# Kernel tuning notes

Hardware: AMD Instinct MI355X
Metric: run time of the kernel (lower is better)

## Reference

```python
import jax, jax.numpy as jnp
import numpy as np

B, N, A = 32, 1024, 256          # batch, n_entities, n_agents
D_IN, D_H, H = 256, 256, 8       # input_dim, hidden_dim, n_heads
SCALE = 1.0 / np.sqrt(D_H)
EPS = 1e-12


def setup_inputs() -> dict:
    key = jax.random.key(0)
    ks = jax.random.split(key, 7)
    x = jax.random.normal(ks[0], (B, N, D_IN), dtype=jnp.float32)
    # binary visibility mask [batch, n_agents, n_entities]
    m = (jax.random.uniform(ks[1], (B, A, N)) > 0.5).astype(jnp.float32)
    # encoder Linear(input_dim, hidden_dim): weight [out,in], bias [out]
    W_enc = jax.random.normal(ks[2], (D_H, D_IN), dtype=jnp.float32) / np.sqrt(D_IN)
    b_enc = jnp.zeros((D_H,), dtype=jnp.float32)
    # per-head projection matrices stacked [H, D_H, D_H] (torch.randn init)
    WQ = jax.random.normal(ks[3], (H, D_H, D_H), dtype=jnp.float32)
    WK = jax.random.normal(ks[4], (H, D_H, D_H), dtype=jnp.float32)
    WV = jax.random.normal(ks[5], (H, D_H, D_H), dtype=jnp.float32)
    return {"x": x, "m": m, "W_enc": W_enc, "b_enc": b_enc, "WQ": WQ, "WK": WK, "WV": WV}


def reference(x, m, W_enc, b_enc, WQ, WK, WV):
    # encode: LeakyReLU then Linear
    h = jnp.einsum('bni,oi->bno', jax.nn.leaky_relu(x), W_enc) + b_enc  # [B,N,D_H]
    n_agents = m.shape[1]
    ha = h[:, :n_agents]                                   # [B,A,D_H]
    # per-head projections, heads vectorized
    Q = jnp.einsum('bad,hde->bhae', ha, WQ)                # [B,H,A,D_H]
    K = jnp.einsum('bnd,hde->bhne', h, WK)                 # [B,H,N,D_H]
    V = jnp.einsum('bnd,hde->bhne', h, WV)                 # [B,H,N,D_H]
    S = jnp.einsum('bhae,bhne->bhan', Q, K) * SCALE        # [B,H,A,N]
    P = jax.nn.softmax(S, axis=-1)
    P = P * m[:, None]                                     # post-softmax mask
    prob = P / (jnp.sum(P, axis=-1, keepdims=True) + EPS)  # renormalize
    z = jnp.einsum('bhan,bhne->bhae', prob, V)             # [B,H,A,D_H]
    return jnp.mean(z, axis=1)                             # [B,A,D_H]
```

## Files before the change

kernel.cpp:

```cpp
#include <hip/hip_runtime.h>
#include <math.h>

namespace {
constexpr int B_N  = 32;
constexpr int SEQ  = 1024;
constexpr int AG   = 256;
constexpr int D    = 256;
constexpr int NH   = 8;
constexpr float SCALE = 0.0625f;
constexpr float EPS   = 1e-12f;

constexpr size_t HHI_OFF  = 0;
constexpr size_t HLO_OFF  = 16777216;
constexpr size_t HT_OFF   = 33554432;
constexpr size_t MTHI_OFF = 50331648;
constexpr size_t MTLO_OFF = 51380224;
constexpr size_t MB_OFF   = 52428800;
constexpr size_t WVT_OFF  = 53477376;
constexpr size_t Z16_OFF  = 54525952;
}

typedef __attribute__((ext_vector_type(8))) short short8;
typedef __attribute__((ext_vector_type(4))) float floatx4;
#define MFMA_BF(A,B,C) __builtin_amdgcn_mfma_f32_16x16x32_bf16(A,B,C,0,0,0)

__device__ __forceinline__ unsigned short bf16_rtne(float f) {
    unsigned u = __float_as_uint(f);
    u += 0x7fffu + ((u >> 16) & 1u);
    return (unsigned short)(u >> 16);
}
__device__ __forceinline__ float bf16_tof(unsigned short h) {
    return __uint_as_float(((unsigned)h) << 16);
}
__device__ __forceinline__ void async16(void* lds, const void* g) {
    __builtin_amdgcn_global_load_lds(
        (const __attribute__((address_space(1))) unsigned int*)g,
        (__attribute__((address_space(3))) unsigned int*)lds,
        16, 0, 0);
}

__global__ __launch_bounds__(256) void enc_kernel(
    const float* __restrict__ x, const float* __restrict__ W_enc,
    const float* __restrict__ b_enc,
    ushort* __restrict__ h_hi, ushort* __restrict__ h_lo)
{
    __shared__ float AsT[32][68];
    __shared__ float BsT[32][68];
    const int t  = threadIdx.x;
    const int tx = t & 15, ty = t >> 4;
    const int col0 = blockIdx.x * 64;
    const int row0 = blockIdx.y * 64;

    float acc[4][4];
#pragma unroll
    for (int r = 0; r < 4; ++r)
#pragma unroll
        for (int c = 0; c < 4; ++c) acc[r][c] = 0.f;

    for (int k0 = 0; k0 < 256; k0 += 32) {
        __syncthreads();
#pragma unroll
        for (int ss = 0; ss < 2; ++ss) {
            int flat = t + 256 * ss;
            int rr = flat >> 3, k4 = flat & 7;
            float4 v = *(const float4*)(x + (size_t)(row0 + rr) * 256 + k0 + k4 * 4);
            v.x = v.x > 0.f ? v.x : 0.01f * v.x;
            v.y = v.y > 0.f ? v.y : 0.01f * v.y;
            v.z = v.z > 0.f ? v.z : 0.01f * v.z;
            v.w = v.w > 0.f ? v.w : 0.01f * v.w;
            AsT[k4*4+0][rr] = v.x; AsT[k4*4+1][rr] = v.y;
            AsT[k4*4+2][rr] = v.z; AsT[k4*4+3][rr] = v.w;
            float4 wv = *(const float4*)(W_enc + (size_t)(col0 + rr) * 256 + k0 + k4 * 4);
            BsT[k4*4+0][rr] = wv.x; BsT[k4*4+1][rr] = wv.y;
            BsT[k4*4+2][rr] = wv.z; BsT[k4*4+3][rr] = wv.w;
        }
        __syncthreads();
#pragma unroll 8
        for (int kk = 0; kk < 32; ++kk) {
            float4 a4 = *(const float4*)&AsT[kk][ty * 4];
            float4 b4 = *(const float4*)&BsT[kk][tx * 4];
            const float ar[4] = {a4.x, a4.y, a4.z, a4.w};
            const float bc[4] = {b4.x, b4.y, b4.z, b4.w};
#pragma unroll
            for (int r = 0; r < 4; ++r)
#pragma unroll
                for (int c = 0; c < 4; ++c)
                    acc[r][c] = fmaf(ar[r], bc[c], acc[r][c]);
        }
    }

    float4 bv = *(const float4*)(b_enc + col0 + tx * 4);
    const float bb4[4] = {bv.x, bv.y, bv.z, bv.w};
#pragma unroll
    for (int r = 0; r < 4; ++r) {
        const int row = row0 + ty * 4 + r;
        ushort hi4[4], lo4[4];
#pragma unroll
        for (int c = 0; c < 4; ++c) {
            float v = acc[r][c] + bb4[c];
            hi4[c] = bf16_rtne(v);
            lo4[c] = bf16_rtne(v - bf16_tof(hi4[c]));
        }
        *(ushort4*)(h_hi + (size_t)row * 256 + col0 + tx * 4) =
            make_ushort4(hi4[0], hi4[1], hi4[2], hi4[3]);
        *(ushort4*)(h_lo + (size_t)row * 256 + col0 + tx * 4) =
            make_ushort4(lo4[0], lo4[1], lo4[2], lo4[3]);
    }
}

__global__ __launch_bounds__(256) void prep_fused(
    const float* __restrict__ m, unsigned* __restrict__ mb,
    const ushort* __restrict__ h_hi, ushort* __restrict__ hT,
    const float* __restrict__ WV, ushort* __restrict__ WVt,
    const float* __restrict__ WQ, const float* __restrict__ WK,
    ushort* __restrict__ Mt_hi, ushort* __restrict__ Mt_lo)
{
    __shared__ __align__(16) char plds[17408];
    const int t = threadIdx.x;
    const int v = blockIdx.x;

    if (v < 1024) {
        const int idx = v * 256 + t;
        const float4* src = (const float4*)(m + (size_t)idx * 32);
        unsigned wbits = 0;
#pragma unroll
        for (int i = 0; i < 8; ++i) {
            float4 vv = src[i];
            wbits |= (vv.x > 0.5f ? 1u : 0u) << (i * 4 + 0);
            wbits |= (vv.y > 0.5f ? 1u : 0u) << (i * 4 + 1);
            wbits |= (vv.z > 0.5f ? 1u : 0u) << (i * 4 + 2);
            wbits |= (vv.w > 0.5f ? 1u : 0u) << (i * 4 + 3);
        }
        mb[idx] = wbits;
    } else if (v < 3072) {
        ushort (*T)[72] = (ushort(*)[72])plds;
        const int v1 = v - 1024;
        const int n0 = (v1 & 15) * 64, d0 = ((v1 >> 4) & 3) * 64, b = v1 >> 6;
        {
            const int r = t >> 2, c = (t & 3) * 16;
            const ushort* src = h_hi + ((size_t)(b * 1024 + n0 + r)) * 256 + d0 + c;
            *(short8*)&T[r][c]     = *(const short8*)src;
            *(short8*)&T[r][c + 8] = *(const short8*)(src + 8);
        }
        __syncthreads();
        {
            const int dd = t >> 2, seg = (t & 3) * 16;
            ushort tmp[16];
#pragma unroll
            for (int j = 0; j < 16; ++j) tmp[j] = T[seg + j][dd];
            ushort* dst = hT + ((size_t)(b * 256 + d0 + dd)) * 1024 + n0 + seg;
            *(short8*)dst       = *(short8*)&tmp[0];
            *(short8*)(dst + 8) = *(short8*)&tmp[8];
        }
    } else if (v < 3200) {
        float (*T)[68] = (float(*)[68])plds;
        const int v2 = v - 3072;
        const int d0 = (v2 & 3) * 64, e0 = ((v2 >> 2) & 3) * 64, h = v2 >> 4;
        {
            const int r = t >> 2, c = (t & 3) * 16;
            const float* src = WV + ((size_t)(h * 256 + d0 + r)) * 256 + e0 + c;
#pragma unroll
            for (int j = 0; j < 4; ++j)
                *(float4*)&T[r][c + j * 4] = *(const float4*)(src + j * 4);
        }
        __syncthreads();
        {
            const int ee = t >> 2, seg = (t & 3) * 16;
            ushort tmp[16];
#pragma unroll
            for (int j = 0; j < 16; ++j) tmp[j] = bf16_rtne(T[seg + j][ee]);
            ushort* dst = WVt + ((size_t)(h * 256 + e0 + ee)) * 256 + d0 + seg;
            *(short8*)dst       = *(short8*)&tmp[0];
            *(short8*)(dst + 8) = *(short8*)&tmp[8];
        }
    } else {
        float (*AsT)[68] = (float(*)[68])plds;
        float (*BsT)[68] = (float(*)[68])(plds + 8704);
        const int v3 = v - 3200;
        const int tx = t & 15, ty = t >> 4;
        const int col0 = (v3 & 3) * 64;
        const int row0 = ((v3 >> 2) & 3) * 64;
        const int hz   = v3 >> 4;
        const float* A  = WK + (size_t)hz * 256 * 256;
        const float* Bm = WQ + (size_t)hz * 256 * 256;
        ushort* Chi = Mt_hi + (size_t)hz * 256 * 256;
        ushort* Clo = Mt_lo + (size_t)hz * 256 * 256;

        float acc[4][4];
#pragma unroll
        for (int r = 0; r < 4; ++r)
#pragma unroll
            for (int c = 0; c < 4; ++c) acc[r][c] = 0.f;

        for (int k0 = 0; k0 < 256; k0 += 32) {
            __syncthreads();
#pragma unroll
            for (int ss = 0; ss < 2; ++ss) {
                int flat = t + 256 * ss;
                int rr = flat >> 3, k4 = flat & 7;
                float4 vv = *(const float4*)(A + (size_t)(row0 + rr) * 256 + k0 + k4 * 4);
                AsT[k4*4+0][rr] = vv.x; AsT[k4*4+1][rr] = vv.y;
                AsT[k4*4+2][rr] = vv.z; AsT[k4*4+3][rr] = vv.w;
                float4 wv = *(const float4*)(Bm + (size_t)(col0 + rr) * 256 + k0 + k4 * 4);
                BsT[k4*4+0][rr] = wv.x; BsT[k4*4+1][rr] = wv.y;
                BsT[k4*4+2][rr] = wv.z; BsT[k4*4+3][rr] = wv.w;
            }
            __syncthreads();
#pragma unroll 8
            for (int kk = 0; kk < 32; ++kk) {
                float4 a4 = *(const float4*)&AsT[kk][ty * 4];
                float4 b4 = *(const float4*)&BsT[kk][tx * 4];
                const float ar[4] = {a4.x, a4.y, a4.z, a4.w};
                const float bc[4] = {b4.x, b4.y, b4.z, b4.w};
#pragma unroll
                for (int r = 0; r < 4; ++r)
#pragma unroll
                    for (int c = 0; c < 4; ++c)
                        acc[r][c] = fmaf(ar[r], bc[c], acc[r][c]);
            }
        }
#pragma unroll
        for (int r = 0; r < 4; ++r) {
            const int row = row0 + ty * 4 + r;
            ushort hi4[4], lo4[4];
#pragma unroll
            for (int c = 0; c < 4; ++c) {
                float vv = acc[r][c];
                hi4[c] = bf16_rtne(vv);
                lo4[c] = bf16_rtne(vv - bf16_tof(hi4[c]));
            }
            *(ushort4*)(Chi + (size_t)row * 256 + col0 + tx * 4) =
                make_ushort4(hi4[0], hi4[1], hi4[2], hi4[3]);
            *(ushort4*)(Clo + (size_t)row * 256 + col0 + tx * 4) =
                make_ushort4(lo4[0], lo4[1], lo4[2], lo4[3]);
        }
    }
}

__global__ __launch_bounds__(512, 2) void attn_mfma(
    const ushort* __restrict__ h_hi, const ushort* __restrict__ h_lo,
    const ushort* __restrict__ hT,   const ushort* __restrict__ Mt_hi,
    const ushort* __restrict__ Mt_lo, const unsigned* __restrict__ mbits,
    ushort* __restrict__ zout)
{
    __shared__ __align__(16) char lds[108544];
    ushort* pP = (ushort*)(lds + 98304);

    const int t    = threadIdx.x;
    const int wv   = t >> 6;
    const int lane = t & 63;
    const int l15  = lane & 15;
    const int quad = lane >> 4;
    const int f    = blockIdx.x;
    const int b    = (f & 7) + 8 * (f >> 7);
    const int mid  = (f >> 3) & 15;
    const int hh   = (mid >> 2) * 2 + (wv >> 2);
    const int a0   = (mid & 3) * 64;
    const int aw   = a0 + (wv & 3) * 16;

    const ushort* hbh = h_hi + (size_t)b * SEQ * D;
    const ushort* hbl = h_lo + (size_t)b * SEQ * D;
    const ushort* hTb = hT   + (size_t)b * D * SEQ;

    floatx4 qac[16];
#pragma unroll
    for (int i = 0; i < 16; ++i) qac[i] = (floatx4){0.f, 0.f, 0.f, 0.f};

    for (int kc = 0; kc < 4; ++kc) {
        short8 Ah[2], Al[2];
#pragma unroll
        for (int kt = 0; kt < 2; ++kt) {
            const size_t ao = ((size_t)b * SEQ + aw + l15) * D +
                              kc * 64 + kt * 32 + quad * 8;
            Ah[kt] = *(const short8*)(h_hi + ao);
            Al[kt] = *(const short8*)(h_lo + ao);
        }
#pragma unroll
        for (int nt2 = 0; nt2 < 16; ++nt2) {
#pragma unroll
            for (int kt = 0; kt < 2; ++kt) {
                const size_t mo = ((size_t)hh * D + nt2 * 16 + l15) * D +
                                  kc * 64 + kt * 32 + quad * 8;
                short8 Bh = *(const short8*)(Mt_hi + mo);
                short8 Bl = *(const short8*)(Mt_lo + mo);
                qac[nt2] = MFMA_BF(Ah[kt], Bh, qac[nt2]);
                qac[nt2] = MFMA_BF(Al[kt], Bh, qac[nt2]);
                qac[nt2] = MFMA_BF(Ah[kt], Bl, qac[nt2]);
            }
        }
    }

    short8 Qhi[8], Qlo[8];
    {
        float* qscr = (float*)lds;
        for (int c = 0; c < 4; ++c) {
#pragma unroll
            for (int j = 0; j < 4; ++j)
#pragma unroll
                for (int r = 0; r < 4; ++r)
                    qscr[(wv * 16 + quad * 4 + r) * 68 + j * 16 + l15] = qac[c * 4 + j][r];
#pragma unroll
            for (int kt = 0; kt < 2; ++kt) {
                const float* pr = &qscr[(wv * 16 + l15) * 68 + kt * 32 + quad * 8];
                float ftmp[8];
                *(float4*)&ftmp[0] = *(const float4*)pr;
                *(float4*)&ftmp[4] = *(const float4*)(pr + 4);
                short8 hi, lo;
#pragma unroll
                for (int e = 0; e < 8; ++e) {
                    unsigned short hb = bf16_rtne(ftmp[e]);
                    hi[e] = (short)hb;
                    lo[e] = (short)bf16_rtne(ftmp[e] - bf16_tof(hb));
                }
                Qhi[c * 2 + kt] = hi;
                Qlo[c * 2 + kt] = lo;
            }
        }
    }
    __syncthreads();

    auto issue_tile = [&](char* buf, int n0) {
        ushort* dh = (ushort*)buf;
        ushort* dl = (ushort*)(buf + 16384);
        ushort* dT = (ushort*)(buf + 32768);
#pragma unroll
        for (int i = 0; i < 2; ++i) {
            const int slot = wv * 128 + i * 64 + lane;
            const int row  = slot >> 5;
            const int p    = slot & 31;
            const int c    = p ^ (row & 7);
            const size_t go = (size_t)(n0 + row) * 256 + c * 8;
            const size_t lo_ = (size_t)(wv * 128 + i * 64) * 8;
            async16(dh + lo_, hbh + go);
            async16(dl + lo_, hbl + go);
        }
#pragma unroll
        for (int i = 0; i < 2; ++i) {
            const int slot = wv * 128 + i * 64 + lane;
            const int row  = slot >> 2;
            const int p    = slot & 3;
            const int c    = p ^ ((row >> 2) & 3);
            async16(dT + (size_t)(wv * 128 + i * 64) * 8,
                    hTb + (size_t)row * 1024 + n0 + c * 8);
        }
    };

    issue_tile(lds,         0);
    issue_tile(lds + 49152, 32);
    __syncthreads();

    floatx4 zac[16];
#pragma unroll
    for (int i = 0; i < 16; ++i) zac[i] = (floatx4){0.f, 0.f, 0.f, 0.f};
    float mx[4] = {-INFINITY, -INFINITY, -INFINITY, -INFINITY};
    float Za[4] = {0.f, 0.f, 0.f, 0.f};
    float Zm[4] = {0.f, 0.f, 0.f, 0.f};

    for (int nt = 0; nt < 32; ++nt) {
        const int n0 = nt * 32;
        char* cur = lds + (size_t)(nt & 1) * 49152;
        ushort* hS_hi = (ushort*)cur;
        ushort* hS_lo = (ushort*)(cur + 16384);
        ushort* hTS   = (ushort*)(cur + 32768);

        floatx4 sac[2];
        sac[0] = (floatx4){0.f, 0.f, 0.f, 0.f};
        sac[1] = (floatx4){0.f, 0.f, 0.f, 0.f};
#pragma unroll
        for (int ks = 0; ks < 8; ++ks) {
            const int cg = ks * 4 + quad;
#pragma unroll
            for (int ntile = 0; ntile < 2; ++ntile) {
                const int row = ntile * 16 + l15;
                const int off = row * 256 + (cg ^ (row & 7)) * 8;
                short8 Bh = *(const short8*)&hS_hi[off];
                short8 Bl = *(const short8*)&hS_lo[off];
                sac[ntile] = MFMA_BF(Qhi[ks], Bh, sac[ntile]);
                sac[ntile] = MFMA_BF(Qlo[ks], Bh, sac[ntile]);
                sac[ntile] = MFMA_BF(Qhi[ks], Bl, sac[ntile]);
            }
        }

        float alr[4];
#pragma unroll
        for (int r = 0; r < 4; ++r) {
            const int a = aw + quad * 4 + r;
            const unsigned w0 = mbits[((size_t)b * AG + a) * (SEQ / 32) + nt];
            float l0 = sac[0][r] * SCALE, l1 = sac[1][r] * SCALE;
            float mt = fmaxf(l0, l1);
#pragma unroll
            for (int off = 1; off < 16; off <<= 1) mt = fmaxf(mt, __shfl_xor(mt, off));
            const float mxn = fmaxf(mx[r], mt);
            const float al  = __expf(mx[r] - mxn);
            float e0 = __expf(l0 - mxn), e1 = __expf(l1 - mxn);
            float p0 = ((w0 >> l15) & 1u)        ? e0 : 0.f;
            float p1 = ((w0 >> (16 + l15)) & 1u) ? e1 : 0.f;
            float za = e0 + e1;
            float zm = p0 + p1;
#pragma unroll
            for (int off = 1; off < 16; off <<= 1) {
                za += __shfl_xor(za, off);
                zm += __shfl_xor(zm, off);
            }
            Za[r] = Za[r] * al + za;
            Zm[r] = Zm[r] * al + zm;
            mx[r] = mxn;
            pP[(wv * 16 + quad * 4 + r) * 40 + l15]      = bf16_rtne(p0);
            pP[(wv * 16 + quad * 4 + r) * 40 + 16 + l15] = bf16_rtne(p1);
            alr[r] = al;
        }
#pragma unroll
        for (int dt = 0; dt < 16; ++dt) {
            zac[dt][0] *= alr[0]; zac[dt][1] *= alr[1];
            zac[dt][2] *= alr[2]; zac[dt][3] *= alr[3];
        }

        short8 Pf = *(const short8*)&pP[(wv * 16 + l15) * 40 + quad * 8];
#pragma unroll
        for (int dt = 0; dt < 16; ++dt) {
            const int row = dt * 16 + l15;
            const int p   = quad ^ ((row >> 2) & 3);
            short8 Bf = *(const short8*)&hTS[row * 32 + p * 8];
            zac[dt] = MFMA_BF(Pf, Bf, zac[dt]);
        }

        __syncthreads();
        if (nt + 2 < 32) issue_tile(cur, (nt + 2) * 32);
    }

#pragma unroll
    for (int r = 0; r < 4; ++r) {
        const int a = aw + quad * 4 + r;
        const float inv = 1.0f / (Zm[r] + EPS * Za[r]);
        ushort* zr = zout + (((size_t)b * NH + hh) * AG + a) * D;
#pragma unroll
        for (int dt = 0; dt < 16; ++dt)
            zr[dt * 16 + l15] = bf16_rtne(zac[dt][r] * inv);
    }
}

__global__ __launch_bounds__(256) void out_mfma(
    const ushort* __restrict__ z16, const ushort* __restrict__ WVt,
    float* __restrict__ out)
{
    const int t    = threadIdx.x;
    const int wv   = t >> 6;
    const int lane = t & 63;
    const int l15  = lane & 15;
    const int quad = lane >> 4;
    const int e0 = blockIdx.x * 64;
    const int a0 = blockIdx.y * 64;
    const int b  = blockIdx.z;
    const int aw = a0 + wv * 16;

    floatx4 acc[4];
#pragma unroll
    for (int i = 0; i < 4; ++i) acc[i] = (floatx4){0.f, 0.f, 0.f, 0.f};

#pragma unroll 4
    for (int c = 0; c < 64; ++c) {
        const int hh = c >> 3, d0 = (c & 7) * 32;
        short8 Af = *(const short8*)(z16 +
            (((size_t)b * NH + hh) * AG + aw + l15) * D + d0 + quad * 8);
#pragma unroll
        for (int et = 0; et < 4; ++et) {
            short8 Bf = *(const short8*)(WVt +
                ((size_t)hh * D + e0 + et * 16 + l15) * D + d0 + quad * 8);
            acc[et] = MFMA_BF(Af, Bf, acc[et]);
        }
    }
#pragma unroll
    for (int et = 0; et < 4; ++et)
#pragma unroll
        for (int r = 0; r < 4; ++r)
            out[((size_t)b * AG + aw + quad * 4 + r) * D + e0 + et * 16 + l15] =
                acc[et][r] * 0.125f;
}

extern "C" void kernel_launch(void* const* d_in, const int* in_sizes, int n_in,
                              void* d_out, int out_size, void* d_ws, size_t ws_size,
                              hipStream_t stream)
{
    (void)in_sizes; (void)n_in; (void)out_size; (void)ws_size;
    const float* x     = (const float*)d_in[0];
    const float* m     = (const float*)d_in[1];
    const float* W_enc = (const float*)d_in[2];
    const float* b_enc = (const float*)d_in[3];
    const float* WQ    = (const float*)d_in[4];
    const float* WK    = (const float*)d_in[5];
    const float* WV    = (const float*)d_in[6];
    float* out = (float*)d_out;
    char* ws = (char*)d_ws;

    ushort*   h_hi  = (ushort*)(ws + HHI_OFF);
    ushort*   h_lo  = (ushort*)(ws + HLO_OFF);
    ushort*   hT    = (ushort*)(ws + HT_OFF);
    ushort*   Mt_hi = (ushort*)(ws + MTHI_OFF);
    ushort*   Mt_lo = (ushort*)(ws + MTLO_OFF);
    unsigned* mbits = (unsigned*)(ws + MB_OFF);
    ushort*   WVt   = (ushort*)(ws + WVT_OFF);
    ushort*   z16   = (ushort*)(ws + Z16_OFF);

    enc_kernel<<<dim3(4, 512, 1), dim3(256), 0, stream>>>(
        x, W_enc, b_enc, h_hi, h_lo);
    prep_fused<<<dim3(3328, 1, 1), dim3(256), 0, stream>>>(
        m, mbits, h_hi, hT, WV, WVt, WQ, WK, Mt_hi, Mt_lo);
    attn_mfma<<<dim3(512, 1, 1), dim3(512), 0, stream>>>(
        h_hi, h_lo, hT, Mt_hi, Mt_lo, mbits, z16);
    out_mfma<<<dim3(4, 4, B_N), dim3(256), 0, stream>>>(z16, WVt, out);
}
```

Baseline: 585.9 us.

## Shrink attention blocks to one head, single-buffer K tile, read hT from global

Each attention block now covers one head with 4 waves (256 threads) instead of two heads with 8 waves, and 1024 blocks are launched. The K tile is single-buffered, and the next tile's load is issued mid-iteration after the score MFMAs. The V-side hT operand is read straight from global memory instead of being staged in LDS. LDS use drops from about 106KB to 37KB so more blocks can be resident, at the cost of uncached global V loads per MFMA and weaker copy/compute overlap.

```diff
diff --git a/kernel.cpp b/kernel.cpp
--- a/kernel.cpp
+++ b/kernel.cpp
@@ -237,14 +237,14 @@
     }
 }
 
-__global__ __launch_bounds__(512, 2) void attn_mfma(
+__global__ __launch_bounds__(256, 3) void attn_mfma(
     const ushort* __restrict__ h_hi, const ushort* __restrict__ h_lo,
     const ushort* __restrict__ hT,   const ushort* __restrict__ Mt_hi,
     const ushort* __restrict__ Mt_lo, const unsigned* __restrict__ mbits,
     ushort* __restrict__ zout)
 {
-    __shared__ __align__(16) char lds[108544];
-    ushort* pP = (ushort*)(lds + 98304);
+    __shared__ __align__(16) char lds[37888];
+    ushort* pP = (ushort*)(lds + 32768);
 
     const int t    = threadIdx.x;
     const int wv   = t >> 6;
@@ -252,11 +252,11 @@
     const int l15  = lane & 15;
     const int quad = lane >> 4;
     const int f    = blockIdx.x;
-    const int b    = (f & 7) + 8 * (f >> 7);
-    const int mid  = (f >> 3) & 15;
-    const int hh   = (mid >> 2) * 2 + (wv >> 2);
-    const int a0   = (mid & 3) * 64;
-    const int aw   = a0 + (wv & 3) * 16;
+    const int b    = (f & 7) + 8 * (f >> 8);
+    const int rk   = (f >> 3) & 31;
+    const int hh   = rk >> 2;
+    const int a0   = (rk & 3) * 64;
+    const int aw   = a0 + wv * 16;
 
     const ushort* hbh = h_hi + (size_t)b * SEQ * D;
     const ushort* hbl = h_lo + (size_t)b * SEQ * D;
@@ -319,34 +319,23 @@
     }
     __syncthreads();
 
-    auto issue_tile = [&](char* buf, int n0) {
-        ushort* dh = (ushort*)buf;
-        ushort* dl = (ushort*)(buf + 16384);
-        ushort* dT = (ushort*)(buf + 32768);
-#pragma unroll
-        for (int i = 0; i < 2; ++i) {
-            const int slot = wv * 128 + i * 64 + lane;
+    auto issue_tile = [&](int n0) {
+        ushort* dh = (ushort*)lds;
+        ushort* dl = (ushort*)(lds + 16384);
+#pragma unroll
+        for (int i = 0; i < 4; ++i) {
+            const int slot = wv * 256 + i * 64 + lane;
             const int row  = slot >> 5;
             const int p    = slot & 31;
             const int c    = p ^ (row & 7);
-            const size_t go = (size_t)(n0 + row) * 256 + c * 8;
-            const size_t lo_ = (size_t)(wv * 128 + i * 64) * 8;
+            const size_t go  = (size_t)(n0 + row) * 256 + c * 8;
+            const size_t lo_ = (size_t)(wv * 256 + i * 64) * 8;
             async16(dh + lo_, hbh + go);
             async16(dl + lo_, hbl + go);
         }
-#pragma unroll
-        for (int i = 0; i < 2; ++i) {
-            const int slot = wv * 128 + i * 64 + lane;
-            const int row  = slot >> 2;
-            const int p    = slot & 3;
-            const int c    = p ^ ((row >> 2) & 3);
-            async16(dT + (size_t)(wv * 128 + i * 64) * 8,
-                    hTb + (size_t)row * 1024 + n0 + c * 8);
-        }
     };
 
-    issue_tile(lds,         0);
-    issue_tile(lds + 49152, 32);
+    issue_tile(0);
     __syncthreads();
 
     floatx4 zac[16];
@@ -356,12 +345,13 @@
     float Za[4] = {0.f, 0.f, 0.f, 0.f};
     float Zm[4] = {0.f, 0.f, 0.f, 0.f};
 
+    const unsigned* mbr = mbits + ((size_t)b * AG + aw + quad * 4) * (SEQ / 32);
+    const ushort*   hTl = hTb + (size_t)l15 * 1024 + quad * 8;
+
     for (int nt = 0; nt < 32; ++nt) {
         const int n0 = nt * 32;
-        char* cur = lds + (size_t)(nt & 1) * 49152;
-        ushort* hS_hi = (ushort*)cur;
-        ushort* hS_lo = (ushort*)(cur + 16384);
-        ushort* hTS   = (ushort*)(cur + 32768);
+        ushort* hS_hi = (ushort*)lds;
+        ushort* hS_lo = (ushort*)(lds + 16384);
 
         floatx4 sac[2];
         sac[0] = (floatx4){0.f, 0.f, 0.f, 0.f};
@@ -381,11 +371,13 @@
             }
         }
 
+        __syncthreads();
+        if (nt + 1 < 32) issue_tile(n0 + 32);
+
         float alr[4];
 #pragma unroll
         for (int r = 0; r < 4; ++r) {
-            const int a = aw + quad * 4 + r;
-            const unsigned w0 = mbits[((size_t)b * AG + a) * (SEQ / 32) + nt];
+            const unsigned w0 = mbr[r * (SEQ / 32) + nt];
             float l0 = sac[0][r] * SCALE, l1 = sac[1][r] * SCALE;
             float mt = fmaxf(l0, l1);
 #pragma unroll
@@ -418,14 +410,11 @@
         short8 Pf = *(const short8*)&pP[(wv * 16 + l15) * 40 + quad * 8];
 #pragma unroll
         for (int dt = 0; dt < 16; ++dt) {
-            const int row = dt * 16 + l15;
-            const int p   = quad ^ ((row >> 2) & 3);
-            short8 Bf = *(const short8*)&hTS[row * 32 + p * 8];
+            short8 Bf = *(const short8*)(hTl + (size_t)dt * 16384 + n0);
             zac[dt] = MFMA_BF(Pf, Bf, zac[dt]);
         }
 
         __syncthreads();
-        if (nt + 2 < 32) issue_tile(cur, (nt + 2) * 32);
     }
 
 #pragma unroll
@@ -505,7 +494,7 @@
         x, W_enc, b_enc, h_hi, h_lo);
     prep_fused<<<dim3(3328, 1, 1), dim3(256), 0, stream>>>(
         m, mbits, h_hi, hT, WV, WVt, WQ, WK, Mt_hi, Mt_lo);
-    attn_mfma<<<dim3(512, 1, 1), dim3(512), 0, stream>>>(
+    attn_mfma<<<dim3(1024, 1, 1), dim3(256), 0, stream>>>(
         h_hi, h_lo, hT, Mt_hi, Mt_lo, mbits, z16);
     out_mfma<<<dim3(4, 4, B_N), dim3(256), 0, stream>>>(z16, WVt, out);
 }
```

New measurement: 1.149 ms. 96.2% more time.

## Use lazy max rescaling and MFMA row sums in masked attention softmax

Applied to the files above, without the earlier changes.

The online softmax now rescales the accumulators only when some row's tile max exceeds the running max by more than a threshold (lazy rescale, checked wave-wide). The per-row shuffle reductions for the masked and unmasked exp sums are replaced by MFMAs against a ones vector, using bf16 P and E tiles staged in extra LDS. The QK score MFMAs are split into two independent accumulator chains to shorten dependency chains. This trades shuffle and rescale ALU work for more LDS (which may lower occupancy) and bf16 rounding in the normalizer sums.

```diff
diff --git a/kernel.cpp b/kernel.cpp
--- a/kernel.cpp
+++ b/kernel.cpp
@@ -243,8 +243,9 @@
     const ushort* __restrict__ Mt_lo, const unsigned* __restrict__ mbits,
     ushort* __restrict__ zout)
 {
-    __shared__ __align__(16) char lds[108544];
+    __shared__ __align__(16) char lds[118784];
     ushort* pP = (ushort*)(lds + 98304);
+    ushort* pE = (ushort*)(lds + 108544);
 
     const int t    = threadIdx.x;
     const int wv   = t >> 6;
@@ -352,20 +353,27 @@
     floatx4 zac[16];
 #pragma unroll
     for (int i = 0; i < 16; ++i) zac[i] = (floatx4){0.f, 0.f, 0.f, 0.f};
+    floatx4 zacZ = (floatx4){0.f, 0.f, 0.f, 0.f};
+    floatx4 zacE = (floatx4){0.f, 0.f, 0.f, 0.f};
     float mx[4] = {-INFINITY, -INFINITY, -INFINITY, -INFINITY};
-    float Za[4] = {0.f, 0.f, 0.f, 0.f};
-    float Zm[4] = {0.f, 0.f, 0.f, 0.f};
+
+    short8 onesf;
+#pragma unroll
+    for (int e = 0; e < 8; ++e) onesf[e] = (short)0x3F80;
+
+    const unsigned* mbr = mbits + ((size_t)b * AG + aw + quad * 4) * (SEQ / 32);
 
     for (int nt = 0; nt < 32; ++nt) {
-        const int n0 = nt * 32;
         char* cur = lds + (size_t)(nt & 1) * 49152;
         ushort* hS_hi = (ushort*)cur;
         ushort* hS_lo = (ushort*)(cur + 16384);
         ushort* hTS   = (ushort*)(cur + 32768);
 
-        floatx4 sac[2];
-        sac[0] = (floatx4){0.f, 0.f, 0.f, 0.f};
-        sac[1] = (floatx4){0.f, 0.f, 0.f, 0.f};
+        floatx4 sacH[2], sacL[2];
+        sacH[0] = (floatx4){0.f, 0.f, 0.f, 0.f};
+        sacH[1] = (floatx4){0.f, 0.f, 0.f, 0.f};
+        sacL[0] = (floatx4){0.f, 0.f, 0.f, 0.f};
+        sacL[1] = (floatx4){0.f, 0.f, 0.f, 0.f};
 #pragma unroll
         for (int ks = 0; ks < 8; ++ks) {
             const int cg = ks * 4 + quad;
@@ -375,47 +383,69 @@
                 const int off = row * 256 + (cg ^ (row & 7)) * 8;
                 short8 Bh = *(const short8*)&hS_hi[off];
                 short8 Bl = *(const short8*)&hS_lo[off];
-                sac[ntile] = MFMA_BF(Qhi[ks], Bh, sac[ntile]);
-                sac[ntile] = MFMA_BF(Qlo[ks], Bh, sac[ntile]);
-                sac[ntile] = MFMA_BF(Qhi[ks], Bl, sac[ntile]);
-            }
-        }
-
-        float alr[4];
+                sacH[ntile] = MFMA_BF(Qhi[ks], Bh, sacH[ntile]);
+                sacL[ntile] = MFMA_BF(Qlo[ks], Bh, sacL[ntile]);
+                sacL[ntile] = MFMA_BF(Qhi[ks], Bl, sacL[ntile]);
+            }
+        }
+
+        float l0[4], l1[4];
 #pragma unroll
         for (int r = 0; r < 4; ++r) {
-            const int a = aw + quad * 4 + r;
-            const unsigned w0 = mbits[((size_t)b * AG + a) * (SEQ / 32) + nt];
-            float l0 = sac[0][r] * SCALE, l1 = sac[1][r] * SCALE;
-            float mt = fmaxf(l0, l1);
-#pragma unroll
-            for (int off = 1; off < 16; off <<= 1) mt = fmaxf(mt, __shfl_xor(mt, off));
-            const float mxn = fmaxf(mx[r], mt);
-            const float al  = __expf(mx[r] - mxn);
-            float e0 = __expf(l0 - mxn), e1 = __expf(l1 - mxn);
-            float p0 = ((w0 >> l15) & 1u)        ? e0 : 0.f;
-            float p1 = ((w0 >> (16 + l15)) & 1u) ? e1 : 0.f;
-            float za = e0 + e1;
-            float zm = p0 + p1;
-#pragma unroll
-            for (int off = 1; off < 16; off <<= 1) {
-                za += __shfl_xor(za, off);
-                zm += __shfl_xor(zm, off);
-            }
-            Za[r] = Za[r] * al + za;
-            Zm[r] = Zm[r] * al + zm;
-            mx[r] = mxn;
-            pP[(wv * 16 + quad * 4 + r) * 40 + l15]      = bf16_rtne(p0);
-            pP[(wv * 16 + quad * 4 + r) * 40 + 16 + l15] = bf16_rtne(p1);
-            alr[r] = al;
-        }
-#pragma unroll
-        for (int dt = 0; dt < 16; ++dt) {
-            zac[dt][0] *= alr[0]; zac[dt][1] *= alr[1];
-            zac[dt][2] *= alr[2]; zac[dt][3] *= alr[3];
+            l0[r] = (sacH[0][r] + sacL[0][r]) * SCALE;
+            l1[r] = (sacH[1][r] + sacL[1][r]) * SCALE;
+        }
+
+        float mt[4];
+#pragma unroll
+        for (int r = 0; r < 4; ++r) mt[r] = fmaxf(l0[r], l1[r]);
+#pragma unroll
+        for (int off = 1; off < 16; off <<= 1) {
+#pragma unroll
+            for (int r = 0; r < 4; ++r)
+                mt[r] = fmaxf(mt[r], __shfl_xor(mt[r], off));
+        }
+
+        const bool need = (mt[0] > mx[0] + 8.0f) || (mt[1] > mx[1] + 8.0f) ||
+                          (mt[2] > mx[2] + 8.0f) || (mt[3] > mx[3] + 8.0f);
+        if (__any(need)) {
+            float alr[4];
+#pragma unroll
+            for (int r = 0; r < 4; ++r) {
+                const float mxn = fmaxf(mx[r], mt[r]);
+                alr[r] = __expf(mx[r] - mxn);
+                mx[r] = mxn;
+            }
+#pragma unroll
+            for (int dt = 0; dt < 16; ++dt) {
+                zac[dt][0] *= alr[0]; zac[dt][1] *= alr[1];
+                zac[dt][2] *= alr[2]; zac[dt][3] *= alr[3];
+            }
+            zacZ[0] *= alr[0]; zacZ[1] *= alr[1];
+            zacZ[2] *= alr[2]; zacZ[3] *= alr[3];
+            zacE[0] *= alr[0]; zacE[1] *= alr[1];
+            zacE[2] *= alr[2]; zacE[3] *= alr[3];
+        }
+
+#pragma unroll
+        for (int r = 0; r < 4; ++r) {
+            const unsigned w0 = mbr[r * (SEQ / 32) + nt];
+            const float e0 = __expf(l0[r] - mx[r]);
+            const float e1 = __expf(l1[r] - mx[r]);
+            const float p0 = ((w0 >> l15) & 1u)        ? e0 : 0.f;
+            const float p1 = ((w0 >> (16 + l15)) & 1u) ? e1 : 0.f;
+            const int row = wv * 16 + quad * 4 + r;
+            pP[row * 40 + l15]      = bf16_rtne(p0);
+            pP[row * 40 + 16 + l15] = bf16_rtne(p1);
+            pE[row * 40 + l15]      = bf16_rtne(e0);
+            pE[row * 40 + 16 + l15] = bf16_rtne(e1);
         }
 
         short8 Pf = *(const short8*)&pP[(wv * 16 + l15) * 40 + quad * 8];
+        short8 Ef = *(const short8*)&pE[(wv * 16 + l15) * 40 + quad * 8];
+        zacZ = MFMA_BF(Pf, onesf, zacZ);
+        zacE = MFMA_BF(Ef, onesf, zacE);
+
 #pragma unroll
         for (int dt = 0; dt < 16; ++dt) {
             const int row = dt * 16 + l15;
@@ -431,7 +461,7 @@
 #pragma unroll
     for (int r = 0; r < 4; ++r) {
         const int a = aw + quad * 4 + r;
-        const float inv = 1.0f / (Zm[r] + EPS * Za[r]);
+        const float inv = 1.0f / (zacZ[r] + EPS * zacE[r]);
         ushort* zr = zout + (((size_t)b * NH + hh) * AG + a) * D;
 #pragma unroll
         for (int dt = 0; dt < 16; ++dt)
```

New measurement: 550.9 us. 6.0% less time.
